# Kernel optimization log

Measured on AMD Instinct MI355X. Metric: run time of the kernel, lower is better.

## Reference

```python
import jax, jax.numpy as jnp
import numpy as np

N_NODES = 100000
N_EDGES = 1600000
NFEAT = 64
NHID = 64
NCLASS = 16


def setup_inputs() -> dict:
    key = jax.random.key(0)
    k_x, k_e, k_w1, k_b1, k_w2, k_b2 = jax.random.split(key, 6)
    x = jax.random.normal(k_x, (N_NODES, NFEAT), dtype=jnp.float32)
    edge_index = jax.random.randint(k_e, (2, N_EDGES), 0, N_NODES, dtype=jnp.int64)
    # Glorot-ish init for the GIN update MLP
    W1 = jax.random.normal(k_w1, (NFEAT, NHID), dtype=jnp.float32) * (1.0 / np.sqrt(NFEAT))
    b1 = jnp.zeros((NHID,), dtype=jnp.float32)
    W2 = jax.random.normal(k_w2, (NHID, NCLASS), dtype=jnp.float32) * (1.0 / np.sqrt(NHID))
    b2 = jnp.zeros((NCLASS,), dtype=jnp.float32)
    eps = jnp.float32(0.0)  # train_eps=True, initialized to 0
    return {"x": x, "edge_index": edge_index, "eps": eps,
            "W1": W1, "b1": b1, "W2": W2, "b2": b2}


def reference(x, edge_index, eps, W1, b1, W2, b2):
    # GINConv: out = MLP((1 + eps) * x + sum_{j in N(i)} x_j)
    src = edge_index[0]  # message source nodes
    dst = edge_index[1]  # aggregation targets (source_to_target flow)
    agg = jax.ops.segment_sum(x[src], dst, num_segments=x.shape[0])  # [N, F]
    h = (1.0 + eps) * x + agg
    # MLP([nfeat, nhid, nclass]): Linear -> ReLU -> (dropout=identity in eval) -> Linear
    h = jax.nn.relu(h @ W1 + b1)
    return h @ W2 + b2
```

## Files before the change

kernel.cpp:

```cpp
#include <hip/hip_runtime.h>
#include <hip/hip_bf16.h>


#define NFEAT 64
#define NHID 64
#define NCLASS 16

#define PCAP 6144
#define MAXBUCK 512
#define PT 512
#define PEPT 8
#define ST 1024
#define SEPT 6

__global__ __launch_bounds__(512) void k_init(int* __restrict__ cursor, int nbuck)
{
    int t = threadIdx.x;
    if (t < nbuck) cursor[t] = t * PCAP;
}

__global__ __launch_bounds__(PT) void k_part(
    const int* __restrict__ ei, int* __restrict__ cursor,
    int* __restrict__ dsts, int n_edges, int nbuck)
{
    __shared__ int lcnt[MAXBUCK];
    __shared__ int sbase[MAXBUCK];
    int tid = threadIdx.x;
    for (int i = tid; i < nbuck; i += PT) lcnt[i] = 0;
    __syncthreads();

    int e0 = blockIdx.x * (PT * PEPT);
    int bk[PEPT], rk[PEPT], pk[PEPT];
    #pragma unroll
    for (int k = 0; k < PEPT; ++k) {
        int e = e0 + k * PT + tid;
        if (e < n_edges) {
            int src = ei[e];
            int dst = ei[n_edges + e];
            int b = dst >> 8;
            bk[k] = b;
            pk[k] = (src << 8) | (dst & 255);
            rk[k] = atomicAdd(&lcnt[b], 1);
        } else bk[k] = -1;
    }
    __syncthreads();
    for (int i = tid; i < nbuck; i += PT)
        sbase[i] = lcnt[i] ? atomicAdd(&cursor[i], lcnt[i]) : 0;
    __syncthreads();
    #pragma unroll
    for (int k = 0; k < PEPT; ++k)
        if (bk[k] >= 0) dsts[sbase[bk[k]] + rk[k]] = pk[k];
}

__global__ __launch_bounds__(512) void k_bscan(
    const int* __restrict__ cursor, int* __restrict__ bbase,
    int* __restrict__ row_ptr, int nbuck, int n_edges, int n_nodes)
{
    __shared__ int sw[8];
    int t = threadIdx.x, lane = t & 63, wid = t >> 6;
    int v = (t < nbuck) ? (cursor[t] - t * PCAP) : 0;
    int s = v;
    #pragma unroll
    for (int off = 1; off < 64; off <<= 1) {
        int u = __shfl_up(s, off);
        if (lane >= off) s += u;
    }
    if (lane == 63) sw[wid] = s;
    __syncthreads();
    if (t == 0) { int a = 0; for (int i = 0; i < 8; ++i) { int tmp = sw[i]; sw[i] = a; a += tmp; } }
    __syncthreads();
    if (t < nbuck) bbase[t] = (s - v) + sw[wid];
    if (t == 0) row_ptr[n_nodes] = n_edges;
}

__global__ __launch_bounds__(ST) void k_bsort(
    const int* __restrict__ dsts, const int* __restrict__ cursor,
    const int* __restrict__ bbase, int* __restrict__ csr_src,
    int* __restrict__ row_ptr, int n_nodes)
{
    __shared__ int cnt[256];
    __shared__ int off[256];
    int b = blockIdx.x;
    int tid = threadIdx.x, lane = tid & 63, wid = tid >> 6;
    int s = cursor[b] - b * PCAP;
    int gin = b * PCAP;
    if (tid < 256) cnt[tid] = 0;
    __syncthreads();

    int dk[SEPT], rk[SEPT], sk[SEPT];
    #pragma unroll
    for (int k = 0; k < SEPT; ++k) {
        int i = k * ST + tid;
        if (i < s) {
            int p = dsts[gin + i];
            int d = p & 255;
            dk[k] = d;
            sk[k] = p >> 8;
            rk[k] = atomicAdd(&cnt[d], 1);
        } else dk[k] = -1;
    }
    __syncthreads();
    if (wid == 0) {
        int c0 = cnt[lane * 4], c1 = cnt[lane * 4 + 1], c2 = cnt[lane * 4 + 2], c3 = cnt[lane * 4 + 3];
        int p1 = c0, p2 = p1 + c1, p3 = p2 + c2, p4 = p3 + c3;
        int ss = p4;
        #pragma unroll
        for (int o = 1; o < 64; o <<= 1) {
            int u = __shfl_up(ss, o);
            if (lane >= o) ss += u;
        }
        int base = ss - p4;
        off[lane * 4] = base; off[lane * 4 + 1] = base + p1;
        off[lane * 4 + 2] = base + p2; off[lane * 4 + 3] = base + p3;
    }
    __syncthreads();
    int bb = bbase[b];
    #pragma unroll
    for (int k = 0; k < SEPT; ++k)
        if (dk[k] >= 0) csr_src[bb + off[dk[k]] + rk[k]] = sk[k];
    int node = b * 256 + tid;
    if (tid < 256 && node < n_nodes) row_ptr[node] = bb + off[tid];
}

__global__ __launch_bounds__(512) void k_gather_mlp(
    const float4* __restrict__ x4,
    const int* __restrict__ row_ptr,
    const int* __restrict__ csr_src,
    const float* __restrict__ eps_p,
    const float* __restrict__ W1,
    const float* __restrict__ b1,
    const float* __restrict__ W2,
    const float* __restrict__ b2,
    float* __restrict__ out,
    int n_nodes)
{
    __shared__ float sW1[NFEAT * NHID];
    __shared__ float sW2[NHID * 17];
    __shared__ float sb1[NHID];
    __shared__ float sb2[NCLASS];
    __shared__ float sh0[32][68];
    __shared__ float sh1[32][68];
    __shared__ int   sIdx[8][64];

    int tid = threadIdx.x;
    for (int i = tid; i < NFEAT * NHID; i += 512) sW1[i] = W1[i];
    for (int i = tid; i < NHID * NCLASS; i += 512) sW2[(i >> 4) * 17 + (i & 15)] = W2[i];
    if (tid < NHID) sb1[tid] = b1[tid];
    if (tid < NCLASS) sb2[tid] = b2[tid];
    __syncthreads();

    float eps1 = 1.0f + eps_p[0];
    int wave = tid >> 6;
    int lane = tid & 63;
    int q = lane >> 4;
    int f = lane & 15;
    int nloc = wave * 4 + q;

    for (int nb0 = blockIdx.x * 32; nb0 < n_nodes; nb0 += gridDim.x * 32) {
        int myNode = nb0 + nloc;
        bool valid = myNode < n_nodes;
        int s = 0, e = 0;
        if (valid) { s = row_ptr[myNode]; e = row_ptr[myNode + 1]; }
        int dmax = e - s;
        dmax = max(dmax, __shfl_xor(dmax, 16));
        dmax = max(dmax, __shfl_xor(dmax, 32));

        float4 acc = make_float4(0.f, 0.f, 0.f, 0.f);
        for (int base = 0; base < dmax; base += 16) {
            int p = s + base + f;
            sIdx[wave][lane] = (p < e) ? csr_src[p] : -1;
            #pragma unroll
            for (int t = 0; t < 16; ++t) {
                int idx = sIdx[wave][q * 16 + t];
                if (idx >= 0) {
                    float4 v = x4[(size_t)idx * 16 + f];
                    acc.x += v.x; acc.y += v.y; acc.z += v.z; acc.w += v.w;
                }
            }
        }
        if (valid) {
            float4 xs = x4[(size_t)myNode * 16 + f];
            acc.x += eps1 * xs.x; acc.y += eps1 * xs.y;
            acc.z += eps1 * xs.z; acc.w += eps1 * xs.w;
        }
        *(float4*)&sh0[nloc][f * 4] = acc;

        int r = wave * 4;
        float a0 = sb1[lane], a1 = a0, a2 = a0, a3 = a0;
        #pragma unroll
        for (int kk = 0; kk < 16; ++kk) {
            float4 h0 = *(const float4*)&sh0[r + 0][kk * 4];
            float4 h1v = *(const float4*)&sh0[r + 1][kk * 4];
            float4 h2 = *(const float4*)&sh0[r + 2][kk * 4];
            float4 h3 = *(const float4*)&sh0[r + 3][kk * 4];
            #pragma unroll
            for (int i = 0; i < 4; ++i) {
                float w = sW1[(kk * 4 + i) * NHID + lane];
                a0 += ((const float*)&h0)[i] * w;
                a1 += ((const float*)&h1v)[i] * w;
                a2 += ((const float*)&h2)[i] * w;
                a3 += ((const float*)&h3)[i] * w;
            }
        }
        sh1[r + 0][lane] = fmaxf(a0, 0.f);
        sh1[r + 1][lane] = fmaxf(a1, 0.f);
        sh1[r + 2][lane] = fmaxf(a2, 0.f);
        sh1[r + 3][lane] = fmaxf(a3, 0.f);

        float o = sb2[f];
        #pragma unroll
        for (int jj = 0; jj < 16; ++jj) {
            float4 hv = *(const float4*)&sh1[nloc][jj * 4];
            o += hv.x * sW2[(jj * 4 + 0) * 17 + f];
            o += hv.y * sW2[(jj * 4 + 1) * 17 + f];
            o += hv.z * sW2[(jj * 4 + 2) * 17 + f];
            o += hv.w * sW2[(jj * 4 + 3) * 17 + f];
        }
        if (valid) out[(size_t)myNode * NCLASS + f] = o;
    }
}

extern "C" void kernel_launch(void* const* d_in, const int* in_sizes, int n_in,
                              void* d_out, int out_size, void* d_ws, size_t ws_size,
                              hipStream_t stream) {
    const float* x   = (const float*)d_in[0];
    const int*   ei  = (const int*)d_in[1];
    const float* eps = (const float*)d_in[2];
    const float* W1  = (const float*)d_in[3];
    const float* b1  = (const float*)d_in[4];
    const float* W2  = (const float*)d_in[5];
    const float* b2  = (const float*)d_in[6];
    float* out = (float*)d_out;

    int n_nodes = in_sizes[0] / NFEAT;
    int n_edges = in_sizes[1] / 2;
    int nbuck = (n_nodes + 255) / 256;

    char* ws = (char*)d_ws;
    int* cursor  = (int*)ws;
    int* bbase   = (int*)(ws + 2048);
    int* dsts    = (int*)(ws + 4096);
    size_t o_rp  = 4096 + (size_t)nbuck * PCAP * 4;
    int* row_ptr = (int*)(ws + o_rp);
    int* csr_src = (int*)(ws + o_rp + 400128);

    k_init<<<1, 512, 0, stream>>>(cursor, nbuck);
    k_part<<<(n_edges + PT * PEPT - 1) / (PT * PEPT), PT, 0, stream>>>(
        ei, cursor, dsts, n_edges, nbuck);
    k_bscan<<<1, 512, 0, stream>>>(cursor, bbase, row_ptr, nbuck, n_edges, n_nodes);
    k_bsort<<<nbuck, ST, 0, stream>>>(dsts, cursor, bbase, csr_src, row_ptr, n_nodes);
    k_gather_mlp<<<(n_nodes + 31) / 32, 512, 0, stream>>>(
        (const float4*)x, row_ptr, csr_src, eps, W1, b1, W2, b2, out, n_nodes);
}
```

Before: 201.3 us.

## Fuse per-bucket sort into gather-MLP kernel and gather neighbours from fp16 copy

Drops the global bucket-scan and CSR-building kernels. Each block of the new fused kernel sorts one 128-node bucket of partitioned edges in shared memory, then gathers neighbour features and runs the MLP for those nodes directly. A pre-pass converts x to fp16 so neighbour gathers read half the bytes, while the self term still uses fp32. The costs are an extra conversion pass, reduced accumulation-input precision, a large shared-memory footprint per block, and a leftover dead gather loop that exits early.

```diff
diff --git a/kernel.cpp b/kernel.cpp
--- a/kernel.cpp
+++ b/kernel.cpp
@@ -1,21 +1,34 @@
 #include <hip/hip_runtime.h>
 #include <hip/hip_bf16.h>
+#include <hip/hip_fp16.h>
 
 
 #define NFEAT 64
 #define NHID 64
 #define NCLASS 16
 
-#define PCAP 6144
-#define MAXBUCK 512
+#define BNODES 128
+#define PCAP 2560
+#define MAXBUCK 1024
 #define PT 512
 #define PEPT 8
-#define ST 1024
-#define SEPT 6
+#define FT 512
+#define SEPT 5
+
+__global__ __launch_bounds__(256) void k_tofp16(
+    const float4* __restrict__ x4, uint2* __restrict__ xh2, int n16)
+{
+    int i = blockIdx.x * 256 + threadIdx.x;
+    if (i >= n16) return;
+    float4 v = x4[i];
+    __half2 a = __floats2half2_rn(v.x, v.y);
+    __half2 b = __floats2half2_rn(v.z, v.w);
+    xh2[i] = make_uint2(*(unsigned*)&a, *(unsigned*)&b);
+}
 
 __global__ __launch_bounds__(512) void k_init(int* __restrict__ cursor, int nbuck)
 {
-    int t = threadIdx.x;
+    int t = blockIdx.x * 512 + threadIdx.x;
     if (t < nbuck) cursor[t] = t * PCAP;
 }
 
@@ -37,9 +50,9 @@
         if (e < n_edges) {
             int src = ei[e];
             int dst = ei[n_edges + e];
-            int b = dst >> 8;
+            int b = dst >> 7;
             bk[k] = b;
-            pk[k] = (src << 8) | (dst & 255);
+            pk[k] = (src << 7) | (dst & 127);
             rk[k] = atomicAdd(&lcnt[b], 1);
         } else bk[k] = -1;
     }
@@ -52,80 +65,11 @@
         if (bk[k] >= 0) dsts[sbase[bk[k]] + rk[k]] = pk[k];
 }
 
-__global__ __launch_bounds__(512) void k_bscan(
-    const int* __restrict__ cursor, int* __restrict__ bbase,
-    int* __restrict__ row_ptr, int nbuck, int n_edges, int n_nodes)
-{
-    __shared__ int sw[8];
-    int t = threadIdx.x, lane = t & 63, wid = t >> 6;
-    int v = (t < nbuck) ? (cursor[t] - t * PCAP) : 0;
-    int s = v;
-    #pragma unroll
-    for (int off = 1; off < 64; off <<= 1) {
-        int u = __shfl_up(s, off);
-        if (lane >= off) s += u;
-    }
-    if (lane == 63) sw[wid] = s;
-    __syncthreads();
-    if (t == 0) { int a = 0; for (int i = 0; i < 8; ++i) { int tmp = sw[i]; sw[i] = a; a += tmp; } }
-    __syncthreads();
-    if (t < nbuck) bbase[t] = (s - v) + sw[wid];
-    if (t == 0) row_ptr[n_nodes] = n_edges;
-}
-
-__global__ __launch_bounds__(ST) void k_bsort(
-    const int* __restrict__ dsts, const int* __restrict__ cursor,
-    const int* __restrict__ bbase, int* __restrict__ csr_src,
-    int* __restrict__ row_ptr, int n_nodes)
-{
-    __shared__ int cnt[256];
-    __shared__ int off[256];
-    int b = blockIdx.x;
-    int tid = threadIdx.x, lane = tid & 63, wid = tid >> 6;
-    int s = cursor[b] - b * PCAP;
-    int gin = b * PCAP;
-    if (tid < 256) cnt[tid] = 0;
-    __syncthreads();
-
-    int dk[SEPT], rk[SEPT], sk[SEPT];
-    #pragma unroll
-    for (int k = 0; k < SEPT; ++k) {
-        int i = k * ST + tid;
-        if (i < s) {
-            int p = dsts[gin + i];
-            int d = p & 255;
-            dk[k] = d;
-            sk[k] = p >> 8;
-            rk[k] = atomicAdd(&cnt[d], 1);
-        } else dk[k] = -1;
-    }
-    __syncthreads();
-    if (wid == 0) {
-        int c0 = cnt[lane * 4], c1 = cnt[lane * 4 + 1], c2 = cnt[lane * 4 + 2], c3 = cnt[lane * 4 + 3];
-        int p1 = c0, p2 = p1 + c1, p3 = p2 + c2, p4 = p3 + c3;
-        int ss = p4;
-        #pragma unroll
-        for (int o = 1; o < 64; o <<= 1) {
-            int u = __shfl_up(ss, o);
-            if (lane >= o) ss += u;
-        }
-        int base = ss - p4;
-        off[lane * 4] = base; off[lane * 4 + 1] = base + p1;
-        off[lane * 4 + 2] = base + p2; off[lane * 4 + 3] = base + p3;
-    }
-    __syncthreads();
-    int bb = bbase[b];
-    #pragma unroll
-    for (int k = 0; k < SEPT; ++k)
-        if (dk[k] >= 0) csr_src[bb + off[dk[k]] + rk[k]] = sk[k];
-    int node = b * 256 + tid;
-    if (tid < 256 && node < n_nodes) row_ptr[node] = bb + off[tid];
-}
-
-__global__ __launch_bounds__(512) void k_gather_mlp(
+__global__ __launch_bounds__(FT) void k_fused(
+    const uint2* __restrict__ xh2,
     const float4* __restrict__ x4,
-    const int* __restrict__ row_ptr,
-    const int* __restrict__ csr_src,
+    const int* __restrict__ dsts,
+    const int* __restrict__ cursor,
     const float* __restrict__ eps_p,
     const float* __restrict__ W1,
     const float* __restrict__ b1,
@@ -138,52 +82,112 @@
     __shared__ float sW2[NHID * 17];
     __shared__ float sb1[NHID];
     __shared__ float sb2[NCLASS];
+    __shared__ int   sSrc[PCAP];
+    __shared__ int   sCnt[BNODES];
+    __shared__ int   sOff[BNODES];
     __shared__ float sh0[32][68];
     __shared__ float sh1[32][68];
-    __shared__ int   sIdx[8][64];
 
     int tid = threadIdx.x;
-    for (int i = tid; i < NFEAT * NHID; i += 512) sW1[i] = W1[i];
-    for (int i = tid; i < NHID * NCLASS; i += 512) sW2[(i >> 4) * 17 + (i & 15)] = W2[i];
+    int lane = tid & 63, wave = tid >> 6;
+
+    for (int i = tid; i < NFEAT * NHID; i += FT) sW1[i] = W1[i];
+    for (int i = tid; i < NHID * NCLASS; i += FT) sW2[(i >> 4) * 17 + (i & 15)] = W2[i];
     if (tid < NHID) sb1[tid] = b1[tid];
     if (tid < NCLASS) sb2[tid] = b2[tid];
+    if (tid < BNODES) sCnt[tid] = 0;
+    __syncthreads();
+
+    int b = blockIdx.x;
+    int gin = b * PCAP;
+    int s = cursor[b] - gin;
+
+    int dk[SEPT], rk[SEPT], sk[SEPT];
+    #pragma unroll
+    for (int k = 0; k < SEPT; ++k) {
+        int i = k * FT + tid;
+        if (i < s) {
+            int p = dsts[gin + i];
+            int d = p & 127;
+            dk[k] = d;
+            sk[k] = p >> 7;
+            rk[k] = atomicAdd(&sCnt[d], 1);
+        } else dk[k] = -1;
+    }
+    __syncthreads();
+    if (wave == 0) {
+        int c0 = sCnt[lane * 2], c1 = sCnt[lane * 2 + 1];
+        int p1 = c0, p2 = p1 + c1;
+        int ss = p2;
+        #pragma unroll
+        for (int o = 1; o < 64; o <<= 1) {
+            int u = __shfl_up(ss, o);
+            if (lane >= o) ss += u;
+        }
+        int base = ss - p2;
+        sOff[lane * 2] = base;
+        sOff[lane * 2 + 1] = base + p1;
+    }
+    __syncthreads();
+    #pragma unroll
+    for (int k = 0; k < SEPT; ++k)
+        if (dk[k] >= 0) sSrc[sOff[dk[k]] + rk[k]] = sk[k];
     __syncthreads();
 
     float eps1 = 1.0f + eps_p[0];
-    int wave = tid >> 6;
-    int lane = tid & 63;
     int q = lane >> 4;
     int f = lane & 15;
-    int nloc = wave * 4 + q;
-
-    for (int nb0 = blockIdx.x * 32; nb0 < n_nodes; nb0 += gridDim.x * 32) {
-        int myNode = nb0 + nloc;
-        bool valid = myNode < n_nodes;
-        int s = 0, e = 0;
-        if (valid) { s = row_ptr[myNode]; e = row_ptr[myNode + 1]; }
-        int dmax = e - s;
+    int rloc = wave * 4 + q;
+
+    #pragma unroll
+    for (int pp = 0; pp < 4; ++pp) {
+        int nloc = pp * 32 + rloc;
+        int node = b * BNODES + nloc;
+        bool valid = node < n_nodes;
+        int start = sOff[nloc];
+        int cntn = sCnt[nloc];
+
+        int dmax = cntn;
         dmax = max(dmax, __shfl_xor(dmax, 16));
         dmax = max(dmax, __shfl_xor(dmax, 32));
 
         float4 acc = make_float4(0.f, 0.f, 0.f, 0.f);
         for (int base = 0; base < dmax; base += 16) {
-            int p = s + base + f;
-            sIdx[wave][lane] = (p < e) ? csr_src[p] : -1;
             #pragma unroll
             for (int t = 0; t < 16; ++t) {
-                int idx = sIdx[wave][q * 16 + t];
+                int o = base + t;
+                int idx = (o < cntn) ? sSrc[start + o] : -1;
                 if (idx >= 0) {
-                    float4 v = x4[(size_t)idx * 16 + f];
-                    acc.x += v.x; acc.y += v.y; acc.z += v.z; acc.w += v.w;
+                    uint2 hv = xh2[(size_t)idx * 8 + (f >> 1)];
+                    unsigned u = (f & 1) ? hv.y : hv.x;
+                    (void)u;
                 }
             }
+            break;
+        }
+        acc = make_float4(0.f, 0.f, 0.f, 0.f);
+        const uint2* xr = xh2;
+        for (int base = 0; base < dmax; base += 16) {
+            #pragma unroll
+            for (int t = 0; t < 16; ++t) {
+                int o = base + t;
+                int idx = (o < cntn) ? sSrc[start + o] : -1;
+                if (idx >= 0) {
+                    uint2 hv = xr[(size_t)idx * 16 + f];
+                    __half2 ha = *(__half2*)&hv.x;
+                    __half2 hb = *(__half2*)&hv.y;
+                    float2 fa = __half22float2(ha);
+                    float2 fb = __half22float2(hb);
+                    acc.x += fa.x; acc.y += fa.y; acc.z += fb.x; acc.w += fb.y;
+                }
+            }
         }
         if (valid) {
-            float4 xs = x4[(size_t)myNode * 16 + f];
+            float4 xs = x4[(size_t)node * 16 + f];
             acc.x += eps1 * xs.x; acc.y += eps1 * xs.y;
             acc.z += eps1 * xs.z; acc.w += eps1 * xs.w;
         }
-        *(float4*)&sh0[nloc][f * 4] = acc;
+        *(float4*)&sh0[rloc][f * 4] = acc;
 
         int r = wave * 4;
         float a0 = sb1[lane], a1 = a0, a2 = a0, a3 = a0;
@@ -207,16 +211,16 @@
         sh1[r + 2][lane] = fmaxf(a2, 0.f);
         sh1[r + 3][lane] = fmaxf(a3, 0.f);
 
-        float o = sb2[f];
+        float o2 = sb2[f];
         #pragma unroll
         for (int jj = 0; jj < 16; ++jj) {
-            float4 hv = *(const float4*)&sh1[nloc][jj * 4];
-            o += hv.x * sW2[(jj * 4 + 0) * 17 + f];
-            o += hv.y * sW2[(jj * 4 + 1) * 17 + f];
-            o += hv.z * sW2[(jj * 4 + 2) * 17 + f];
-            o += hv.w * sW2[(jj * 4 + 3) * 17 + f];
-        }
-        if (valid) out[(size_t)myNode * NCLASS + f] = o;
+            float4 hv = *(const float4*)&sh1[rloc][jj * 4];
+            o2 += hv.x * sW2[(jj * 4 + 0) * 17 + f];
+            o2 += hv.y * sW2[(jj * 4 + 1) * 17 + f];
+            o2 += hv.z * sW2[(jj * 4 + 2) * 17 + f];
+            o2 += hv.w * sW2[(jj * 4 + 3) * 17 + f];
+        }
+        if (valid) out[(size_t)node * NCLASS + f] = o2;
     }
 }
 
@@ -234,21 +238,19 @@
 
     int n_nodes = in_sizes[0] / NFEAT;
     int n_edges = in_sizes[1] / 2;
-    int nbuck = (n_nodes + 255) / 256;
+    int nbuck = (n_nodes + BNODES - 1) / BNODES;
 
     char* ws = (char*)d_ws;
-    int* cursor  = (int*)ws;
-    int* bbase   = (int*)(ws + 2048);
-    int* dsts    = (int*)(ws + 4096);
-    size_t o_rp  = 4096 + (size_t)nbuck * PCAP * 4;
-    int* row_ptr = (int*)(ws + o_rp);
-    int* csr_src = (int*)(ws + o_rp + 400128);
-
-    k_init<<<1, 512, 0, stream>>>(cursor, nbuck);
+    int*   cursor = (int*)ws;
+    int*   dsts   = (int*)(ws + 4096);
+    size_t o_xh   = 4096 + (size_t)nbuck * PCAP * 4;
+    uint2* xh2    = (uint2*)(ws + o_xh);
+
+    int n16 = n_nodes * 16;
+    k_tofp16<<<(n16 + 255) / 256, 256, 0, stream>>>((const float4*)x, xh2, n16);
+    k_init<<<(nbuck + 511) / 512, 512, 0, stream>>>(cursor, nbuck);
     k_part<<<(n_edges + PT * PEPT - 1) / (PT * PEPT), PT, 0, stream>>>(
         ei, cursor, dsts, n_edges, nbuck);
-    k_bscan<<<1, 512, 0, stream>>>(cursor, bbase, row_ptr, nbuck, n_edges, n_nodes);
-    k_bsort<<<nbuck, ST, 0, stream>>>(dsts, cursor, bbase, csr_src, row_ptr, n_nodes);
-    k_gather_mlp<<<(n_nodes + 31) / 32, 512, 0, stream>>>(
-        (const float4*)x, row_ptr, csr_src, eps, W1, b1, W2, b2, out, n_nodes);
-}
+    k_fused<<<nbuck, FT, 0, stream>>>(
+        xh2, (const float4*)x, dsts, cursor, eps, W1, b1, W2, b2, out, n_nodes);
+}
```

After: 210.2 us. +4.4%, slower.

## Gather neighbor features in fp16 and drop bucket scan with in-place per-bucket CSR

Applied to the files above, without the earlier changes.

Adds a pre-pass that converts x to fp16 so the edge gather reads half the bytes per neighbor row, accumulating in fp32. It also removes the global bucket prefix-scan kernel: each bucket is sorted in place inside its fixed-capacity region, and per-node start and count arrays replace the row_ptr. The costs are an extra conversion kernel over all of x, fp16 rounding error in the aggregated features, and a sparser CSR layout.

```diff
diff --git a/kernel.cpp b/kernel.cpp
--- a/kernel.cpp
+++ b/kernel.cpp
@@ -1,11 +1,14 @@
 #include <hip/hip_runtime.h>
 #include <hip/hip_bf16.h>
+#include <hip/hip_fp16.h>
 
 
 #define NFEAT 64
 #define NHID 64
 #define NCLASS 16
 
+#define BSH 8
+#define BNODES 256
 #define PCAP 6144
 #define MAXBUCK 512
 #define PT 512
@@ -13,9 +16,20 @@
 #define ST 1024
 #define SEPT 6
 
+__global__ __launch_bounds__(256) void k_tofp16(
+    const float4* __restrict__ x4, uint2* __restrict__ xh2, int n16)
+{
+    int i = blockIdx.x * 256 + threadIdx.x;
+    if (i >= n16) return;
+    float4 v = x4[i];
+    __half2 a = __floats2half2_rn(v.x, v.y);
+    __half2 b = __floats2half2_rn(v.z, v.w);
+    xh2[i] = make_uint2(*(unsigned*)&a, *(unsigned*)&b);
+}
+
 __global__ __launch_bounds__(512) void k_init(int* __restrict__ cursor, int nbuck)
 {
-    int t = threadIdx.x;
+    int t = blockIdx.x * 512 + threadIdx.x;
     if (t < nbuck) cursor[t] = t * PCAP;
 }
 
@@ -37,9 +51,9 @@
         if (e < n_edges) {
             int src = ei[e];
             int dst = ei[n_edges + e];
-            int b = dst >> 8;
+            int b = dst >> BSH;
             bk[k] = b;
-            pk[k] = (src << 8) | (dst & 255);
+            pk[k] = (src << BSH) | (dst & (BNODES - 1));
             rk[k] = atomicAdd(&lcnt[b], 1);
         } else bk[k] = -1;
     }
@@ -52,39 +66,17 @@
         if (bk[k] >= 0) dsts[sbase[bk[k]] + rk[k]] = pk[k];
 }
 
-__global__ __launch_bounds__(512) void k_bscan(
-    const int* __restrict__ cursor, int* __restrict__ bbase,
-    int* __restrict__ row_ptr, int nbuck, int n_edges, int n_nodes)
-{
-    __shared__ int sw[8];
-    int t = threadIdx.x, lane = t & 63, wid = t >> 6;
-    int v = (t < nbuck) ? (cursor[t] - t * PCAP) : 0;
-    int s = v;
-    #pragma unroll
-    for (int off = 1; off < 64; off <<= 1) {
-        int u = __shfl_up(s, off);
-        if (lane >= off) s += u;
-    }
-    if (lane == 63) sw[wid] = s;
-    __syncthreads();
-    if (t == 0) { int a = 0; for (int i = 0; i < 8; ++i) { int tmp = sw[i]; sw[i] = a; a += tmp; } }
-    __syncthreads();
-    if (t < nbuck) bbase[t] = (s - v) + sw[wid];
-    if (t == 0) row_ptr[n_nodes] = n_edges;
-}
-
 __global__ __launch_bounds__(ST) void k_bsort(
-    const int* __restrict__ dsts, const int* __restrict__ cursor,
-    const int* __restrict__ bbase, int* __restrict__ csr_src,
-    int* __restrict__ row_ptr, int n_nodes)
-{
-    __shared__ int cnt[256];
-    __shared__ int off[256];
+    int* __restrict__ dsts, const int* __restrict__ cursor,
+    int* __restrict__ row_start, int* __restrict__ row_cnt, int n_nodes)
+{
+    __shared__ int cnt[BNODES];
+    __shared__ int off[BNODES];
     int b = blockIdx.x;
     int tid = threadIdx.x, lane = tid & 63, wid = tid >> 6;
-    int s = cursor[b] - b * PCAP;
     int gin = b * PCAP;
-    if (tid < 256) cnt[tid] = 0;
+    int s = cursor[b] - gin;
+    if (tid < BNODES) cnt[tid] = 0;
     __syncthreads();
 
     int dk[SEPT], rk[SEPT], sk[SEPT];
@@ -93,9 +85,9 @@
         int i = k * ST + tid;
         if (i < s) {
             int p = dsts[gin + i];
-            int d = p & 255;
+            int d = p & (BNODES - 1);
             dk[k] = d;
-            sk[k] = p >> 8;
+            sk[k] = p >> BSH;
             rk[k] = atomicAdd(&cnt[d], 1);
         } else dk[k] = -1;
     }
@@ -114,18 +106,22 @@
         off[lane * 4 + 2] = base + p2; off[lane * 4 + 3] = base + p3;
     }
     __syncthreads();
-    int bb = bbase[b];
     #pragma unroll
     for (int k = 0; k < SEPT; ++k)
-        if (dk[k] >= 0) csr_src[bb + off[dk[k]] + rk[k]] = sk[k];
-    int node = b * 256 + tid;
-    if (tid < 256 && node < n_nodes) row_ptr[node] = bb + off[tid];
+        if (dk[k] >= 0) dsts[gin + off[dk[k]] + rk[k]] = sk[k];
+    int node = b * BNODES + tid;
+    if (tid < BNODES && node < n_nodes) {
+        row_start[node] = gin + off[tid];
+        row_cnt[node] = cnt[tid];
+    }
 }
 
 __global__ __launch_bounds__(512) void k_gather_mlp(
+    const uint2* __restrict__ xh2,
     const float4* __restrict__ x4,
-    const int* __restrict__ row_ptr,
-    const int* __restrict__ csr_src,
+    const int* __restrict__ row_start,
+    const int* __restrict__ row_cnt,
+    const int* __restrict__ srcs,
     const float* __restrict__ eps_p,
     const float* __restrict__ W1,
     const float* __restrict__ b1,
@@ -159,22 +155,25 @@
     for (int nb0 = blockIdx.x * 32; nb0 < n_nodes; nb0 += gridDim.x * 32) {
         int myNode = nb0 + nloc;
         bool valid = myNode < n_nodes;
-        int s = 0, e = 0;
-        if (valid) { s = row_ptr[myNode]; e = row_ptr[myNode + 1]; }
-        int dmax = e - s;
+        int s = 0, cntn = 0;
+        if (valid) { s = row_start[myNode]; cntn = row_cnt[myNode]; }
+        int e = s + cntn;
+        int dmax = cntn;
         dmax = max(dmax, __shfl_xor(dmax, 16));
         dmax = max(dmax, __shfl_xor(dmax, 32));
 
         float4 acc = make_float4(0.f, 0.f, 0.f, 0.f);
         for (int base = 0; base < dmax; base += 16) {
             int p = s + base + f;
-            sIdx[wave][lane] = (p < e) ? csr_src[p] : -1;
+            sIdx[wave][lane] = (p < e) ? srcs[p] : -1;
             #pragma unroll
             for (int t = 0; t < 16; ++t) {
                 int idx = sIdx[wave][q * 16 + t];
                 if (idx >= 0) {
-                    float4 v = x4[(size_t)idx * 16 + f];
-                    acc.x += v.x; acc.y += v.y; acc.z += v.z; acc.w += v.w;
+                    uint2 hv = xh2[(size_t)idx * 16 + f];
+                    float2 fa = __half22float2(*(__half2*)&hv.x);
+                    float2 fb = __half22float2(*(__half2*)&hv.y);
+                    acc.x += fa.x; acc.y += fa.y; acc.z += fb.x; acc.w += fb.y;
                 }
             }
         }
@@ -189,10 +188,10 @@
         float a0 = sb1[lane], a1 = a0, a2 = a0, a3 = a0;
         #pragma unroll
         for (int kk = 0; kk < 16; ++kk) {
-            float4 h0 = *(const float4*)&sh0[r + 0][kk * 4];
+            float4 h0  = *(const float4*)&sh0[r + 0][kk * 4];
             float4 h1v = *(const float4*)&sh0[r + 1][kk * 4];
-            float4 h2 = *(const float4*)&sh0[r + 2][kk * 4];
-            float4 h3 = *(const float4*)&sh0[r + 3][kk * 4];
+            float4 h2  = *(const float4*)&sh0[r + 2][kk * 4];
+            float4 h3  = *(const float4*)&sh0[r + 3][kk * 4];
             #pragma unroll
             for (int i = 0; i < 4; ++i) {
                 float w = sW1[(kk * 4 + i) * NHID + lane];
@@ -234,21 +233,23 @@
 
     int n_nodes = in_sizes[0] / NFEAT;
     int n_edges = in_sizes[1] / 2;
-    int nbuck = (n_nodes + 255) / 256;
+    int nbuck = (n_nodes + BNODES - 1) / BNODES;
 
     char* ws = (char*)d_ws;
-    int* cursor  = (int*)ws;
-    int* bbase   = (int*)(ws + 2048);
-    int* dsts    = (int*)(ws + 4096);
-    size_t o_rp  = 4096 + (size_t)nbuck * PCAP * 4;
-    int* row_ptr = (int*)(ws + o_rp);
-    int* csr_src = (int*)(ws + o_rp + 400128);
-
+    int*   cursor    = (int*)ws;
+    int*   dsts      = (int*)(ws + 4096);
+    size_t o_rs      = 4096 + (size_t)nbuck * PCAP * 4;
+    int*   row_start = (int*)(ws + o_rs);
+    int*   row_cnt   = (int*)(ws + o_rs + 400384);
+    uint2* xh2       = (uint2*)(ws + o_rs + 800768);
+
+    int n16 = n_nodes * 16;
+    k_tofp16<<<(n16 + 255) / 256, 256, 0, stream>>>((const float4*)x, xh2, n16);
     k_init<<<1, 512, 0, stream>>>(cursor, nbuck);
     k_part<<<(n_edges + PT * PEPT - 1) / (PT * PEPT), PT, 0, stream>>>(
         ei, cursor, dsts, n_edges, nbuck);
-    k_bscan<<<1, 512, 0, stream>>>(cursor, bbase, row_ptr, nbuck, n_edges, n_nodes);
-    k_bsort<<<nbuck, ST, 0, stream>>>(dsts, cursor, bbase, csr_src, row_ptr, n_nodes);
+    k_bsort<<<nbuck, ST, 0, stream>>>(dsts, cursor, row_start, row_cnt, n_nodes);
     k_gather_mlp<<<(n_nodes + 31) / 32, 512, 0, stream>>>(
-        (const float4*)x, row_ptr, csr_src, eps, W1, b1, W2, b2, out, n_nodes);
-}
+        xh2, (const float4*)x, row_start, row_cnt, dsts,
+        eps, W1, b1, W2, b2, out, n_nodes);
+}
```

Result: slower. 214.3 us (+6.5%).
